# Performance work log

Measured on AMD Instinct MI355X. Metric: run time of the kernel, lower is better.

The kernel has to match this reference:

```python
import jax, jax.numpy as jnp
import numpy as np

N = 100000
E = 1600000
IN_F = 128
OUT_F = 32
HEADS = 6
NEG_SLOPE = 0.2


def setup_inputs() -> dict:
    key = jax.random.key(0)
    k1, k2, k3, k4, k5 = jax.random.split(key, 5)
    x = jax.random.normal(k1, (N, IN_F), dtype=jnp.float32)
    edge_index = jax.random.randint(k2, (2, E), 0, N, dtype=jnp.int64)
    # GATConv params (PyG layout): shared linear for src/dst, per-head attention vectors, bias
    glorot = lambda k, shape: jax.random.normal(k, shape, dtype=jnp.float32) * np.sqrt(2.0 / (shape[0] + shape[-1]))
    W = glorot(k3, (IN_F, HEADS * OUT_F))          # lin.weight^T
    att_src = glorot(k4, (HEADS, OUT_F)) * 0.1     # [H, C]
    att_dst = glorot(k5, (HEADS, OUT_F)) * 0.1
    bias = jnp.zeros((OUT_F,), dtype=jnp.float32)  # concat=False -> bias of size out_feature
    return {"x": x, "edge_index": edge_index, "W": W,
            "att_src": att_src, "att_dst": att_dst, "bias": bias}


def reference(x, edge_index, W, att_src, att_dst, bias):
    src, dst = edge_index[0], edge_index[1]
    # Linear projection to per-head features: [N, H, C]
    xp = (x @ W).reshape(N, HEADS, OUT_F)
    # Per-node attention logit halves: [N, H]
    a_s = jnp.einsum("nhc,hc->nh", xp, att_src)
    a_d = jnp.einsum("nhc,hc->nh", xp, att_dst)
    # Per-edge logits with LeakyReLU: [E, H]
    e = jax.nn.leaky_relu(a_s[src] + a_d[dst], negative_slope=NEG_SLOPE)
    # Segment softmax over edges grouped by destination node
    m = jax.ops.segment_max(e, dst, num_segments=N)            # [N, H]
    m = jnp.where(jnp.isfinite(m), m, 0.0)                     # empty segments -> -inf guard
    e = jnp.exp(e - m[dst])
    s = jax.ops.segment_sum(e, dst, num_segments=N)            # [N, H]
    alpha = e / (s[dst] + 1e-16)                               # [E, H]
    # Weighted scatter-add aggregation: [N, H, C]
    msg = xp[src] * alpha[:, :, None]
    out = jax.ops.segment_sum(msg, dst, num_segments=N)
    # concat=False -> mean over heads, add bias, then SELU
    out = out.mean(axis=1) + bias
    return jax.nn.selu(out)
```

## Files before the change

kernel.cpp:

```cpp
#include <hip/hip_runtime.h>


typedef __attribute__((ext_vector_type(8))) short short8;
typedef __attribute__((ext_vector_type(4))) float f32x4;

#define SK 136
#define SP 200

__device__ __forceinline__ unsigned short f2bf(float f)
{
    unsigned int u = __float_as_uint(f);
    u = (u + 0x7fffu + ((u >> 16) & 1u)) >> 16;
    return (unsigned short)u;
}
__device__ __forceinline__ float bf2f(unsigned int lo16)
{
    return __uint_as_float(lo16 << 16);
}

__global__ __launch_bounds__(256) void k_gemm(
    const float* __restrict__ x, const float* __restrict__ W,
    const float* __restrict__ att_src, const float* __restrict__ att_dst,
    unsigned short* __restrict__ xpb, float* __restrict__ a_s, float* __restrict__ a_d,
    int N)
{
    __shared__ __align__(16) unsigned short smem[64 * SP];
    __shared__ float s_att[2][192];
    const int t    = threadIdx.x;
    const int wave = t >> 6;
    const int lane = t & 63;
    const int ln   = lane & 15;
    const int q    = lane >> 4;
    const int n0   = blockIdx.x * 64;
    const int cb   = wave * 48;

    if (t < 192) {
        s_att[0][t] = att_src[t];
        s_att[1][t] = att_dst[t];
    }

    {
        const float4* x4 = (const float4*)x;
        #pragma unroll
        for (int it = 0; it < 8; ++it) {
            int i   = t + it * 256;
            int row = i >> 5;
            int c4  = i & 31;
            int gr  = n0 + row;
            if (gr > N - 1) gr = N - 1;
            float4 f = x4[(size_t)gr * 32 + c4];
            unsigned int u0 = (unsigned int)f2bf(f.x) | ((unsigned int)f2bf(f.y) << 16);
            unsigned int u1 = (unsigned int)f2bf(f.z) | ((unsigned int)f2bf(f.w) << 16);
            *(uint2*)(smem + row * SK + c4 * 4) = make_uint2(u0, u1);
        }
    }

    short8 bw[3][4];
    #pragma unroll
    for (int nt = 0; nt < 3; ++nt)
        #pragma unroll
        for (int kbi = 0; kbi < 4; ++kbi) {
            short8 v;
            #pragma unroll
            for (int j = 0; j < 8; ++j) {
                int k = kbi * 32 + q * 8 + j;
                v[j] = (short)f2bf(W[k * 192 + cb + nt * 16 + ln]);
            }
            bw[nt][kbi] = v;
        }

    __syncthreads();

    f32x4 acc[4][3];
    #pragma unroll
    for (int mt = 0; mt < 4; ++mt)
        #pragma unroll
        for (int nt = 0; nt < 3; ++nt) acc[mt][nt] = (f32x4)0.f;

    #pragma unroll
    for (int kbi = 0; kbi < 4; ++kbi) {
        #pragma unroll
        for (int mt = 0; mt < 4; ++mt) {
            short8 av = *(const short8*)(smem + (mt * 16 + ln) * SK + kbi * 32 + q * 8);
            #pragma unroll
            for (int nt = 0; nt < 3; ++nt)
                acc[mt][nt] = __builtin_amdgcn_mfma_f32_16x16x32_bf16(
                    av, bw[nt][kbi], acc[mt][nt], 0, 0, 0);
        }
    }

    __syncthreads();

    #pragma unroll
    for (int mt = 0; mt < 4; ++mt) {
        #pragma unroll
        for (int r = 0; r < 4; ++r) {
            int row  = mt * 16 + q * 4 + r;
            int grow = n0 + row;
            #pragma unroll
            for (int nt = 0; nt < 3; ++nt) {
                unsigned short b = f2bf(acc[mt][nt][r]);
                smem[row * SP + cb + nt * 16 + ln] = b;
                if (grow < N)
                    xpb[(size_t)grow * 192 + cb + nt * 16 + ln] = b;
            }
        }
    }

    __syncthreads();

    #pragma unroll
    for (int id = t; id < 384; id += 256) {
        int row = id / 6, h = id - row * 6;
        int gn = n0 + row;
        if (gn < N) {
            const unsigned int* p32 = (const unsigned int*)(smem + row * SP + h * 32);
            float s = 0.f, d = 0.f;
            #pragma unroll
            for (int u = 0; u < 16; ++u) {
                unsigned int v = p32[u];
                float x0 = bf2f(v & 0xffffu);
                float x1 = bf2f(v >> 16);
                s = fmaf(x0, s_att[0][h * 32 + u * 2], s);
                s = fmaf(x1, s_att[0][h * 32 + u * 2 + 1], s);
                d = fmaf(x0, s_att[1][h * 32 + u * 2], d);
                d = fmaf(x1, s_att[1][h * 32 + u * 2 + 1], d);
            }
            a_s[(size_t)gn * 6 + h] = s;
            a_d[(size_t)gn * 6 + h] = d;
        }
    }
}

__global__ void k_deg(const int* __restrict__ ei, int* __restrict__ deg,
                      int* __restrict__ rank, int E)
{
    int e = blockIdx.x * blockDim.x + threadIdx.x;
    if (e < E) rank[e] = atomicAdd(&deg[ei[E + e]], 1);
}

__global__ __launch_bounds__(256) void k_bsum(
    const int* __restrict__ deg, int* __restrict__ bsum, int N)
{
    __shared__ int sd[256];
    const int b = blockIdx.x, t = threadIdx.x;
    const int base = b * 1024;
    int s = 0;
    #pragma unroll
    for (int k = 0; k < 4; ++k) {
        int g = base + t + k * 256;
        if (g < N) s += deg[g];
    }
    sd[t] = s;
    __syncthreads();
    for (int o = 128; o; o >>= 1) {
        if (t < o) sd[t] += sd[t + o];
        __syncthreads();
    }
    if (t == 0) bsum[b] = sd[0];
}

__global__ __launch_bounds__(256) void k_off(
    const int* __restrict__ deg, const int* __restrict__ bsum,
    int* __restrict__ off, int N, int NB)
{
    __shared__ int sw[256];
    __shared__ int sbase;
    const int b = blockIdx.x, t = threadIdx.x;

    sw[t] = (t < b) ? bsum[t] : 0;
    __syncthreads();
    for (int o = 128; o; o >>= 1) {
        if (t < o) sw[t] += sw[t + o];
        __syncthreads();
    }
    if (t == 0) sbase = sw[0];
    __syncthreads();

    const int base = b * 1024 + t * 4;
    int d[4]; int s = 0;
    #pragma unroll
    for (int k = 0; k < 4; ++k) {
        int g = base + k;
        d[k] = (g < N) ? deg[g] : 0;
        s += d[k];
    }
    sw[t] = s;
    __syncthreads();
    for (int o = 1; o < 256; o <<= 1) {
        int add = (t >= o) ? sw[t - o] : 0;
        __syncthreads();
        sw[t] += add;
        __syncthreads();
    }
    int run = sbase + (sw[t] - s);
    #pragma unroll
    for (int k = 0; k < 4; ++k) {
        int g = base + k;
        if (g < N) off[g] = run;
        run += d[k];
    }
    if (b == NB - 1 && t == 255) off[N] = sbase + sw[255];
}

__global__ void k_scat(const int* __restrict__ ei, const int* __restrict__ off,
                       const int* __restrict__ rank, int* __restrict__ csr_src, int E)
{
    int e = blockIdx.x * blockDim.x + threadIdx.x;
    if (e < E) {
        int dst = ei[E + e];
        csr_src[off[dst] + rank[e]] = ei[e];
    }
}

__global__ __launch_bounds__(256) void k_agg(
    const unsigned short* __restrict__ xpb,
    const float* __restrict__ a_s, const float* __restrict__ a_d,
    const int* __restrict__ csr_src, const int* __restrict__ off,
    const float* __restrict__ bias, float* __restrict__ out, int N)
{
    const int wid = threadIdx.x >> 6;
    const int l   = threadIdx.x & 63;
    const int n = blockIdx.x * 4 + wid;
    if (n >= N) return;

    const int nb  = off[n];
    const int deg = off[n + 1] - nb;
    const int hr  = l >> 3;
    const int h   = hr < 6 ? hr : 5;
    const int lc  = l < 48 ? l : 47;
    const unsigned lcb = (unsigned)lc * 8u;
    const unsigned h4  = (unsigned)h * 4u;
    const char* __restrict__ xpB = (const char*)xpb;
    const char* __restrict__ asB = (const char*)a_s;

    const float zd = a_d[(size_t)n * 6 + h];

    float ax = 0.f, ay = 0.f, az = 0.f, aw = 0.f, se = 0.f;

    if (deg <= 64) {
        int my3 = (l < deg) ? csr_src[nb + l] * 3 : 0;
        int i = 0;
        for (; i + 8 <= deg; i += 8) {
            unsigned s3[8]; float as[8]; uint2 xv[8];
            #pragma unroll
            for (int k = 0; k < 8; ++k) {
                s3[k] = (unsigned)__shfl(my3, i + k);
                as[k] = *(const float*)(asB + s3[k] * 8u + h4);
            }
            #pragma unroll
            for (int k = 0; k < 8; ++k)
                xv[k] = *(const uint2*)(xpB + s3[k] * 128u + lcb);
            #pragma unroll
            for (int k = 0; k < 8; ++k) {
                float z = as[k] + zd;
                z = z > 0.f ? z : 0.2f * z;
                float ev = __expf(z);
                ax = fmaf(ev, __uint_as_float(xv[k].x << 16), ax);
                ay = fmaf(ev, __uint_as_float(xv[k].x & 0xffff0000u), ay);
                az = fmaf(ev, __uint_as_float(xv[k].y << 16), az);
                aw = fmaf(ev, __uint_as_float(xv[k].y & 0xffff0000u), aw);
                se += ev;
            }
        }
        for (; i < deg; ++i) {
            unsigned s3 = (unsigned)__shfl(my3, i);
            float z  = *(const float*)(asB + s3 * 8u + h4) + zd;
            z = z > 0.f ? z : 0.2f * z;
            float ev = __expf(z);
            uint2 xv = *(const uint2*)(xpB + s3 * 128u + lcb);
            ax = fmaf(ev, __uint_as_float(xv.x << 16), ax);
            ay = fmaf(ev, __uint_as_float(xv.x & 0xffff0000u), ay);
            az = fmaf(ev, __uint_as_float(xv.y << 16), az);
            aw = fmaf(ev, __uint_as_float(xv.y & 0xffff0000u), aw);
            se += ev;
        }
    } else {
        int i = 0;
        for (; i + 4 <= deg; i += 4) {
            unsigned s3[4]; float as[4]; uint2 xv[4];
            #pragma unroll
            for (int k = 0; k < 4; ++k) {
                s3[k] = (unsigned)csr_src[nb + i + k] * 3u;
                as[k] = *(const float*)(asB + s3[k] * 8u + h4);
            }
            #pragma unroll
            for (int k = 0; k < 4; ++k)
                xv[k] = *(const uint2*)(xpB + s3[k] * 128u + lcb);
            #pragma unroll
            for (int k = 0; k < 4; ++k) {
                float z = as[k] + zd;
                z = z > 0.f ? z : 0.2f * z;
                float ev = __expf(z);
                ax = fmaf(ev, __uint_as_float(xv[k].x << 16), ax);
                ay = fmaf(ev, __uint_as_float(xv[k].x & 0xffff0000u), ay);
                az = fmaf(ev, __uint_as_float(xv[k].y << 16), az);
                aw = fmaf(ev, __uint_as_float(xv[k].y & 0xffff0000u), aw);
                se += ev;
            }
        }
        for (; i < deg; ++i) {
            unsigned s3 = (unsigned)csr_src[nb + i] * 3u;
            float z  = *(const float*)(asB + s3 * 8u + h4) + zd;
            z = z > 0.f ? z : 0.2f * z;
            float ev = __expf(z);
            uint2 xv = *(const uint2*)(xpB + s3 * 128u + lcb);
            ax = fmaf(ev, __uint_as_float(xv.x << 16), ax);
            ay = fmaf(ev, __uint_as_float(xv.x & 0xffff0000u), ay);
            az = fmaf(ev, __uint_as_float(xv.y << 16), az);
            aw = fmaf(ev, __uint_as_float(xv.y & 0xffff0000u), aw);
            se += ev;
        }
    }

    const float inv = 1.f / (se + 1e-16f);
    float v0 = (l < 48) ? ax * inv : 0.f;
    float v1 = (l < 48) ? ay * inv : 0.f;
    float v2 = (l < 48) ? az * inv : 0.f;
    float v3 = (l < 48) ? aw * inv : 0.f;

    #pragma unroll
    for (int d = 8; d <= 32; d <<= 1) {
        v0 += __shfl_down(v0, d);
        v1 += __shfl_down(v1, d);
        v2 += __shfl_down(v2, d);
        v3 += __shfl_down(v3, d);
    }

    if (l < 8) {
        float4 b4 = ((const float4*)bias)[l];
        const float sc = 1.0507009873554805f, al = 1.6732632423543772f;
        float m[4] = {v0 * (1.f / 6.f) + b4.x, v1 * (1.f / 6.f) + b4.y,
                      v2 * (1.f / 6.f) + b4.z, v3 * (1.f / 6.f) + b4.w};
        #pragma unroll
        for (int k = 0; k < 4; ++k)
            m[k] = m[k] > 0.f ? sc * m[k] : sc * al * (__expf(m[k]) - 1.f);
        ((float4*)out)[(size_t)n * 8 + l] = make_float4(m[0], m[1], m[2], m[3]);
    }
}

extern "C" void kernel_launch(void* const* d_in, const int* in_sizes, int n_in,
                              void* d_out, int out_size, void* d_ws, size_t ws_size,
                              hipStream_t stream)
{
    const float* x       = (const float*)d_in[0];
    const int*   ei      = (const int*)d_in[1];
    const float* W       = (const float*)d_in[2];
    const float* att_src = (const float*)d_in[3];
    const float* att_dst = (const float*)d_in[4];
    const float* bias    = (const float*)d_in[5];
    float* out = (float*)d_out;

    const int N = in_sizes[0] / 128;
    const int E = in_sizes[1] / 2;
    const int NB = (N + 1023) / 1024;

    char* ws = (char*)d_ws;
    size_t o = 0;
    auto take = [&](size_t bytes) { size_t r = o; o = (o + bytes + 255) & ~(size_t)255; return r; };
    unsigned short* xpb = (unsigned short*)(ws + take((size_t)N * 192 * 2));
    float* a_s     = (float*)(ws + take((size_t)N * 6 * 4));
    float* a_d     = (float*)(ws + take((size_t)N * 6 * 4));
    int*   off     = (int*)  (ws + take((size_t)(N + 1) * 4));
    int*   deg     = (int*)  (ws + take((size_t)N * 4));
    int*   rank    = (int*)  (ws + take((size_t)E * 4));
    int*   csr_src = (int*)  (ws + take((size_t)E * 4));
    int*   bsum    = (int*)  (ws + take((size_t)NB * 4));
    (void)ws_size; (void)n_in; (void)out_size;

    hipMemsetAsync(deg, 0, (size_t)N * 4, stream);

    k_gemm<<<(N + 63) / 64, 256, 0, stream>>>(x, W, att_src, att_dst,
                                              xpb, a_s, a_d, N);
    int eg = (E + 255) / 256;
    k_deg<<<eg, 256, 0, stream>>>(ei, deg, rank, E);
    k_bsum<<<NB, 256, 0, stream>>>(deg, bsum, N);
    k_off<<<NB, 256, 0, stream>>>(deg, bsum, off, N, NB);
    k_scat<<<eg, 256, 0, stream>>>(ei, off, rank, csr_src, E);
    k_agg<<<(N + 3) / 4, 256, 0, stream>>>(xpb, a_s, a_d, csr_src, off, bias, out, N);
}
```

Baseline: 316.8 us.

## Fold attention vectors into projection weights and pad aggregation tails

```diff
diff --git a/kernel.cpp b/kernel.cpp
--- a/kernel.cpp
+++ b/kernel.cpp
@@ -5,7 +5,6 @@
 typedef __attribute__((ext_vector_type(4))) float f32x4;
 
 #define SK 136
-#define SP 200
 
 __device__ __forceinline__ unsigned short f2bf(float f)
 {
@@ -13,19 +12,33 @@
     u = (u + 0x7fffu + ((u >> 16) & 1u)) >> 16;
     return (unsigned short)u;
 }
-__device__ __forceinline__ float bf2f(unsigned int lo16)
-{
-    return __uint_as_float(lo16 << 16);
+
+__global__ __launch_bounds__(256) void k_watt(
+    const float* __restrict__ W,
+    const float* __restrict__ att_src, const float* __restrict__ att_dst,
+    unsigned short* __restrict__ wat)
+{
+    int i = blockIdx.x * 256 + threadIdx.x;
+    if (i >= 128 * 16) return;
+    int k = i >> 4, c = i & 15;
+    float v = 0.f;
+    if (c < 12) {
+        int h = c < 6 ? c : c - 6;
+        const float* av = (c < 6 ? att_src : att_dst) + h * 32;
+        const float* wr = W + k * 192 + h * 32;
+        #pragma unroll
+        for (int j = 0; j < 32; ++j) v = fmaf(wr[j], av[j], v);
+    }
+    wat[i] = f2bf(v);
 }
 
 __global__ __launch_bounds__(256) void k_gemm(
     const float* __restrict__ x, const float* __restrict__ W,
-    const float* __restrict__ att_src, const float* __restrict__ att_dst,
+    const unsigned short* __restrict__ wat,
     unsigned short* __restrict__ xpb, float* __restrict__ a_s, float* __restrict__ a_d,
     int N)
 {
-    __shared__ __align__(16) unsigned short smem[64 * SP];
-    __shared__ float s_att[2][192];
+    __shared__ __align__(16) unsigned short xt[64 * SK];
     const int t    = threadIdx.x;
     const int wave = t >> 6;
     const int lane = t & 63;
@@ -33,11 +46,6 @@
     const int q    = lane >> 4;
     const int n0   = blockIdx.x * 64;
     const int cb   = wave * 48;
-
-    if (t < 192) {
-        s_att[0][t] = att_src[t];
-        s_att[1][t] = att_dst[t];
-    }
 
     {
         const float4* x4 = (const float4*)x;
@@ -51,7 +59,7 @@
             float4 f = x4[(size_t)gr * 32 + c4];
             unsigned int u0 = (unsigned int)f2bf(f.x) | ((unsigned int)f2bf(f.y) << 16);
             unsigned int u1 = (unsigned int)f2bf(f.z) | ((unsigned int)f2bf(f.w) << 16);
-            *(uint2*)(smem + row * SK + c4 * 4) = make_uint2(u0, u1);
+            *(uint2*)(xt + row * SK + c4 * 4) = make_uint2(u0, u1);
         }
     }
 
@@ -69,65 +77,67 @@
             bw[nt][kbi] = v;
         }
 
+    short8 bwa[4];
+    if (wave == 0) {
+        #pragma unroll
+        for (int kbi = 0; kbi < 4; ++kbi) {
+            short8 v;
+            #pragma unroll
+            for (int j = 0; j < 8; ++j)
+                v[j] = (short)wat[(kbi * 32 + q * 8 + j) * 16 + ln];
+            bwa[kbi] = v;
+        }
+    }
+
     __syncthreads();
 
     f32x4 acc[4][3];
-    #pragma unroll
-    for (int mt = 0; mt < 4; ++mt)
+    f32x4 acca[4];
+    #pragma unroll
+    for (int mt = 0; mt < 4; ++mt) {
+        acca[mt] = (f32x4)0.f;
         #pragma unroll
         for (int nt = 0; nt < 3; ++nt) acc[mt][nt] = (f32x4)0.f;
+    }
 
     #pragma unroll
     for (int kbi = 0; kbi < 4; ++kbi) {
         #pragma unroll
         for (int mt = 0; mt < 4; ++mt) {
-            short8 av = *(const short8*)(smem + (mt * 16 + ln) * SK + kbi * 32 + q * 8);
+            short8 av = *(const short8*)(xt + (mt * 16 + ln) * SK + kbi * 32 + q * 8);
             #pragma unroll
             for (int nt = 0; nt < 3; ++nt)
                 acc[mt][nt] = __builtin_amdgcn_mfma_f32_16x16x32_bf16(
                     av, bw[nt][kbi], acc[mt][nt], 0, 0, 0);
-        }
-    }
-
-    __syncthreads();
+            if (wave == 0)
+                acca[mt] = __builtin_amdgcn_mfma_f32_16x16x32_bf16(
+                    av, bwa[kbi], acca[mt], 0, 0, 0);
+        }
+    }
 
     #pragma unroll
     for (int mt = 0; mt < 4; ++mt) {
         #pragma unroll
         for (int r = 0; r < 4; ++r) {
-            int row  = mt * 16 + q * 4 + r;
-            int grow = n0 + row;
-            #pragma unroll
-            for (int nt = 0; nt < 3; ++nt) {
-                unsigned short b = f2bf(acc[mt][nt][r]);
-                smem[row * SP + cb + nt * 16 + ln] = b;
-                if (grow < N)
-                    xpb[(size_t)grow * 192 + cb + nt * 16 + ln] = b;
-            }
-        }
-    }
-
-    __syncthreads();
-
-    #pragma unroll
-    for (int id = t; id < 384; id += 256) {
-        int row = id / 6, h = id - row * 6;
-        int gn = n0 + row;
-        if (gn < N) {
-            const unsigned int* p32 = (const unsigned int*)(smem + row * SP + h * 32);
-            float s = 0.f, d = 0.f;
-            #pragma unroll
-            for (int u = 0; u < 16; ++u) {
-                unsigned int v = p32[u];
-                float x0 = bf2f(v & 0xffffu);
-                float x1 = bf2f(v >> 16);
-                s = fmaf(x0, s_att[0][h * 32 + u * 2], s);
-                s = fmaf(x1, s_att[0][h * 32 + u * 2 + 1], s);
-                d = fmaf(x0, s_att[1][h * 32 + u * 2], d);
-                d = fmaf(x1, s_att[1][h * 32 + u * 2 + 1], d);
-            }
-            a_s[(size_t)gn * 6 + h] = s;
-            a_d[(size_t)gn * 6 + h] = d;
+            int grow = n0 + mt * 16 + q * 4 + r;
+            if (grow < N) {
+                #pragma unroll
+                for (int nt = 0; nt < 3; ++nt)
+                    xpb[(size_t)grow * 192 + cb + nt * 16 + ln] = f2bf(acc[mt][nt][r]);
+            }
+        }
+    }
+    if (wave == 0) {
+        #pragma unroll
+        for (int mt = 0; mt < 4; ++mt) {
+            #pragma unroll
+            for (int r = 0; r < 4; ++r) {
+                int grow = n0 + mt * 16 + q * 4 + r;
+                if (grow < N) {
+                    if (ln < 6)       a_s[(size_t)grow * 6 + ln]     = acca[mt][r];
+                    else if (ln < 12) a_d[(size_t)grow * 6 + ln - 6] = acca[mt][r];
+                }
+            }
         }
     }
 }
@@ -240,12 +250,15 @@
 
     if (deg <= 64) {
         int my3 = (l < deg) ? csr_src[nb + l] * 3 : 0;
-        int i = 0;
-        for (; i + 8 <= deg; i += 8) {
+        const int nch = (deg + 7) >> 3;
+        for (int ch = 0; ch < nch; ++ch) {
+            const int base = ch * 8;
             unsigned s3[8]; float as[8]; uint2 xv[8];
             #pragma unroll
             for (int k = 0; k < 8; ++k) {
-                s3[k] = (unsigned)__shfl(my3, i + k);
+                int idx = base + k;
+                int sl  = idx < deg ? idx : deg - 1;
+                s3[k] = (unsigned)__shfl(my3, sl);
                 as[k] = *(const float*)(asB + s3[k] * 8u + h4);
             }
             #pragma unroll
@@ -253,7 +266,7 @@
                 xv[k] = *(const uint2*)(xpB + s3[k] * 128u + lcb);
             #pragma unroll
             for (int k = 0; k < 8; ++k) {
-                float z = as[k] + zd;
+                float z = (base + k < deg) ? as[k] + zd : -1e4f;
                 z = z > 0.f ? z : 0.2f * z;
                 float ev = __expf(z);
                 ax = fmaf(ev, __uint_as_float(xv[k].x << 16), ax);
@@ -263,25 +276,16 @@
                 se += ev;
             }
         }
-        for (; i < deg; ++i) {
-            unsigned s3 = (unsigned)__shfl(my3, i);
-            float z  = *(const float*)(asB + s3 * 8u + h4) + zd;
-            z = z > 0.f ? z : 0.2f * z;
-            float ev = __expf(z);
-            uint2 xv = *(const uint2*)(xpB + s3 * 128u + lcb);
-            ax = fmaf(ev, __uint_as_float(xv.x << 16), ax);
-            ay = fmaf(ev, __uint_as_float(xv.x & 0xffff0000u), ay);
-            az = fmaf(ev, __uint_as_float(xv.y << 16), az);
-            aw = fmaf(ev, __uint_as_float(xv.y & 0xffff0000u), aw);
-            se += ev;
-        }
     } else {
-        int i = 0;
-        for (; i + 4 <= deg; i += 4) {
+        const int nch = (deg + 3) >> 2;
+        for (int ch = 0; ch < nch; ++ch) {
+            const int base = ch * 4;
             unsigned s3[4]; float as[4]; uint2 xv[4];
             #pragma unroll
             for (int k = 0; k < 4; ++k) {
-                s3[k] = (unsigned)csr_src[nb + i + k] * 3u;
+                int idx = base + k;
+                int ic  = idx < deg ? idx : deg - 1;
+                s3[k] = (unsigned)csr_src[nb + ic] * 3u;
                 as[k] = *(const float*)(asB + s3[k] * 8u + h4);
             }
             #pragma unroll
@@ -289,7 +293,7 @@
                 xv[k] = *(const uint2*)(xpB + s3[k] * 128u + lcb);
             #pragma unroll
             for (int k = 0; k < 4; ++k) {
-                float z = as[k] + zd;
+                float z = (base + k < deg) ? as[k] + zd : -1e4f;
                 z = z > 0.f ? z : 0.2f * z;
                 float ev = __expf(z);
                 ax = fmaf(ev, __uint_as_float(xv[k].x << 16), ax);
@@ -298,18 +302,6 @@
                 aw = fmaf(ev, __uint_as_float(xv[k].y & 0xffff0000u), aw);
                 se += ev;
             }
-        }
-        for (; i < deg; ++i) {
-            unsigned s3 = (unsigned)csr_src[nb + i] * 3u;
-            float z  = *(const float*)(asB + s3 * 8u + h4) + zd;
-            z = z > 0.f ? z : 0.2f * z;
-            float ev = __expf(z);
-            uint2 xv = *(const uint2*)(xpB + s3 * 128u + lcb);
-            ax = fmaf(ev, __uint_as_float(xv.x << 16), ax);
-            ay = fmaf(ev, __uint_as_float(xv.x & 0xffff0000u), ay);
-            az = fmaf(ev, __uint_as_float(xv.y << 16), az);
-            aw = fmaf(ev, __uint_as_float(xv.y & 0xffff0000u), aw);
-            se += ev;
         }
     }
 
@@ -366,12 +358,13 @@
     int*   rank    = (int*)  (ws + take((size_t)E * 4));
     int*   csr_src = (int*)  (ws + take((size_t)E * 4));
     int*   bsum    = (int*)  (ws + take((size_t)NB * 4));
+    unsigned short* wat = (unsigned short*)(ws + take((size_t)128 * 16 * 2));
     (void)ws_size; (void)n_in; (void)out_size;
 
     hipMemsetAsync(deg, 0, (size_t)N * 4, stream);
 
-    k_gemm<<<(N + 63) / 64, 256, 0, stream>>>(x, W, att_src, att_dst,
-                                              xpb, a_s, a_d, N);
+    k_watt<<<8, 256, 0, stream>>>(W, att_src, att_dst, wat);
+    k_gemm<<<(N + 63) / 64, 256, 0, stream>>>(x, W, wat, xpb, a_s, a_d, N);
     int eg = (E + 255) / 256;
     k_deg<<<eg, 256, 0, stream>>>(ei, deg, rank, E);
     k_bsum<<<NB, 256, 0, stream>>>(deg, bsum, N);
```

Result: slower. 349.3 us (+10.2%).
